# Optimization experiments

Hardware: AMD Instinct MI355X
Metric: run time of the kernel (lower is better)

## Reference

```python
import jax, jax.numpy as jnp
import numpy as np
import math
from jax import lax

B, C, H, DK, L, K, NCONV, P = 24, 128, 8, 16, 512, 7, 4, 0.1


def setup_inputs() -> dict:
    key = jax.random.key(0)
    ks = jax.random.split(key, 10)
    return {
        "x": jax.random.normal(ks[0], (B, C, L), jnp.float32),
        "dw_w": jax.random.normal(ks[1], (NCONV, C, 1, K), jnp.float32) * 0.1,
        "dw_b": jax.random.normal(ks[2], (NCONV, C), jnp.float32) * 0.1,
        "pw_w": jax.random.normal(ks[3], (NCONV, C, C, 1), jnp.float32) * 0.05,
        "pw_b": jax.random.normal(ks[4], (NCONV, C), jnp.float32) * 0.1,
        "Wq": jax.random.normal(ks[5], (H, B, DK, C), jnp.float32),
        "Wk": jax.random.normal(ks[6], (H, B, DK, C), jnp.float32),
        "Wv": jax.random.normal(ks[7], (H, B, DK, C), jnp.float32),
        "Wo": jax.random.normal(ks[8], (B, C, C), jnp.float32),
        "W": jax.random.normal(ks[9], (B, C, C), jnp.float32),
    }


def _norm(t, eps=1e-6):
    # torch: (x - mean) / (std + eps), std unbiased (ddof=1), over last (length) axis
    mean = t.mean(-1, keepdims=True)
    std = jnp.sqrt(((t - mean) ** 2).sum(-1, keepdims=True) / (t.shape[-1] - 1))
    return (t - mean) / (std + eps)


def _dropout(t, i):
    # deterministic dropout (training=True, p=0.1) with fixed per-call key
    keep = jax.random.bernoulli(jax.random.fold_in(jax.random.key(7), i), 1.0 - P, t.shape)
    return jnp.where(keep, t / (1.0 - P), jnp.zeros((), t.dtype))


def reference(x, dw_w, dw_b, pw_w, pw_b, Wq, Wk, Wv, Wo, W):
    # positional encoding: sin(sin(pos*freq + phase)) + x (note the double sin, faithful to source)
    i = np.arange(C)
    base = 10000.0 ** (-(i - (i % 2)) / C)
    freq = jnp.asarray(np.where(i % 2 == 0, base, -base), jnp.float32)
    phase = jnp.asarray(np.where(i % 2 == 0, 0.0, np.pi / 2), jnp.float32)
    pos = jnp.arange(L, dtype=jnp.float32)
    pe = jnp.sin(jnp.sin(pos[None, :] * freq[:, None] + phase[:, None]))  # (C, L)
    out = pe[None] + x
    res = out
    dn = ('NCH', 'OIH', 'NCH')
    for ci in range(NCONV):
        o = _norm(out)
        o = lax.conv_general_dilated(o, dw_w[ci], (1,), [(K // 2, K // 2)],
                                     feature_group_count=C, dimension_numbers=dn) + dw_b[ci][None, :, None]
        o = lax.conv_general_dilated(o, pw_w[ci], (1,), [(0, 0)],
                                     dimension_numbers=dn) + pw_b[ci][None, :, None]
        o = jax.nn.relu(o)
        out = _dropout(res + o, ci)
        res = out
    # self-attention (per-batch-element weight matrices, softmax over QUERY axis = torch dim=1)
    xn = _norm(out)
    q = jnp.einsum('hbkc,bcl->hbkl', Wq, xn)
    k = jnp.einsum('hbkc,bcl->hbkl', Wk, xn)
    v = jnp.einsum('hbkc,bcl->hbkl', Wv, xn)
    s = jnp.einsum('hbki,hbkj->hbij', q, k) / math.sqrt(DK)  # (H,B,L,L)
    p = jax.nn.softmax(s, axis=2)
    head = jnp.einsum('hbvi,hbij->hbvj', v, p)  # (H,B,DK,L)
    head = head.transpose(1, 0, 2, 3).reshape(B, H * DK, L)
    att = jnp.einsum('boc,bcl->bol', Wo, head)
    out = _dropout(res + att, NCONV)
    res = out
    # final per-batch projection + relu + residual
    o = jax.nn.relu(jnp.einsum('boc,bcl->bol', W, _norm(out)))
    out = _dropout(res + o, NCONV + 1)
    return out
```

## Files before the change

kernel.cpp:

```cpp
#include <hip/hip_runtime.h>
#include <stdint.h>
#include <math.h>

#define NB 24
#define NC 128
#define NH 8
#define NDK 16
#define NL 512
#define NTOT (24*128*512)

typedef float f32x4 __attribute__((ext_vector_type(4)));
typedef short s16x4 __attribute__((ext_vector_type(4)));

__device__ inline f32x4 mfma_bf16_16x16x16(s16x4 a, s16x4 b, f32x4 c) {
#if defined(__HIP_DEVICE_COMPILE__)
#if __has_builtin(__builtin_amdgcn_mfma_f32_16x16x16bf16_1k)
  return __builtin_amdgcn_mfma_f32_16x16x16bf16_1k(a, b, c, 0, 0, 0);
#else
  return __builtin_amdgcn_mfma_f32_16x16x16_bf16(a, b, c, 0, 0, 0);
#endif
#else
  (void)a; (void)b;
  return c;
#endif
}

__device__ inline unsigned short f2bf(float x) {
  uint32_t u = __float_as_uint(x);
  return (unsigned short)((u + 0x7FFFu + ((u >> 16) & 1u)) >> 16);
}
__device__ inline float bf2f(unsigned short s) {
  return __uint_as_float(((uint32_t)s) << 16);
}

__host__ __device__ inline void tf2x32(uint32_t k0, uint32_t k1, uint32_t& x0, uint32_t& x1) {
  uint32_t ks2 = k0 ^ k1 ^ 0x1BD11BDAu;
  x0 += k0; x1 += k1;
#define TF_R(r) { x0 += x1; x1 = (x1 << r) | (x1 >> (32 - r)); x1 ^= x0; }
  TF_R(13) TF_R(15) TF_R(26) TF_R(6)
  x0 += k1;  x1 += ks2 + 1u;
  TF_R(17) TF_R(29) TF_R(16) TF_R(24)
  x0 += ks2; x1 += k0 + 2u;
  TF_R(13) TF_R(15) TF_R(26) TF_R(6)
  x0 += k0;  x1 += k1 + 3u;
  TF_R(17) TF_R(29) TF_R(16) TF_R(24)
  x0 += k1;  x1 += ks2 + 4u;
  TF_R(13) TF_R(15) TF_R(26) TF_R(6)
  x0 += ks2; x1 += k0 + 5u;
#undef TF_R
}

__device__ inline float drop_scale(uint32_t k0, uint32_t k1, uint32_t idx) {
  uint32_t x0 = 0u, x1 = idx;
  tf2x32(k0, k1, x0, x1);
  uint32_t bits = x0 ^ x1;
  float u = __uint_as_float((bits >> 9) | 0x3f800000u) - 1.0f;
  return (u < 0.9f) ? (1.0f / 0.9f) : 0.0f;
}

#define S0 (4*128*128)
#define SW (24*128*128)
#define SQ (8*24*16*128)
#define oPwH 0
#define oPwL (S0)
#define oWoH (2*S0)
#define oWoL (2*S0 + SW)
#define oWH  (2*S0 + 2*SW)
#define oWL  (2*S0 + 3*SW)
#define oQH  (2*S0 + 4*SW)
#define oQL  (2*S0 + 4*SW + SQ)
#define oKH  (2*S0 + 4*SW + 2*SQ)
#define oKL  (2*S0 + 4*SW + 3*SQ)
#define oVH  (2*S0 + 4*SW + 4*SQ)
#define oVL  (2*S0 + 4*SW + 5*SQ)
#define PREP_TOT (S0 + 2*SW + 3*SQ)

__global__ __launch_bounds__(256) void prep_split_kernel(
    const float* __restrict__ pw_w, const float* __restrict__ Wo, const float* __restrict__ W,
    const float* __restrict__ Wq, const float* __restrict__ Wk, const float* __restrict__ Wv,
    unsigned short* __restrict__ ws) {
  int idx = blockIdx.x * 256 + threadIdx.x;
  const float* src; unsigned short *dh, *dl; int off;
  if (idx < S0)                { src = pw_w; dh = ws + oPwH; dl = ws + oPwL; off = idx; }
  else if (idx < S0 + SW)      { src = Wo;   dh = ws + oWoH; dl = ws + oWoL; off = idx - S0; }
  else if (idx < S0 + 2*SW)    { src = W;    dh = ws + oWH;  dl = ws + oWL;  off = idx - S0 - SW; }
  else if (idx < S0 + 2*SW + SQ)   { src = Wq; dh = ws + oQH; dl = ws + oQL; off = idx - S0 - 2*SW; }
  else if (idx < S0 + 2*SW + 2*SQ) { src = Wk; dh = ws + oKH; dl = ws + oKL; off = idx - S0 - 2*SW - SQ; }
  else                             { src = Wv; dh = ws + oVH; dl = ws + oVL; off = idx - S0 - 2*SW - 2*SQ; }
  float v = src[off];
  unsigned short hi = f2bf(v);
  dh[off] = hi;
  dl[off] = f2bf(v - bf2f(hi));
}

template<bool DO_CONV, bool ADD_PE>
__global__ __launch_bounds__(64) void norm_dw_kernel(const float* __restrict__ in,
                                                     float* __restrict__ cur_out,
                                                     unsigned short* __restrict__ oh,
                                                     unsigned short* __restrict__ ol,
                                                     const float* __restrict__ dww,
                                                     const float* __restrict__ dwb) {
  int row = blockIdx.x;
  int c = row & (NC - 1);
  int t = threadIdx.x;
  const float* rp = in + (size_t)row * NL;
  float4 v0 = ((const float4*)rp)[t * 2];
  float4 v1 = ((const float4*)rp)[t * 2 + 1];
  float xr[8] = {v0.x, v0.y, v0.z, v0.w, v1.x, v1.y, v1.z, v1.w};
  if (ADD_PE) {
    int ce = c & ~1;
    double base = exp(-(double)ce * 9.210340371976184 / 128.0);
    float freq = (c & 1) ? -(float)base : (float)base;
    float phase = (c & 1) ? (float)(M_PI / 2.0) : 0.0f;
#pragma unroll
    for (int j = 0; j < 8; ++j)
      xr[j] += sinf(sinf((float)(t * 8 + j) * freq + phase));
    float4 o0 = make_float4(xr[0], xr[1], xr[2], xr[3]);
    float4 o1 = make_float4(xr[4], xr[5], xr[6], xr[7]);
    float4* cp = (float4*)(cur_out + (size_t)row * NL);
    cp[t * 2] = o0; cp[t * 2 + 1] = o1;
  }
  float s = 0.f;
#pragma unroll
  for (int j = 0; j < 8; ++j) s += xr[j];
#pragma unroll
  for (int off = 32; off >= 1; off >>= 1) s += __shfl_xor(s, off);
  float mean = s * (1.0f / 512.0f);
  float sq = 0.f;
#pragma unroll
  for (int j = 0; j < 8; ++j) { xr[j] -= mean; sq += xr[j] * xr[j]; }
#pragma unroll
  for (int off = 32; off >= 1; off >>= 1) sq += __shfl_xor(sq, off);
  float inv = 1.0f / (sqrtf(sq * (1.0f / 511.0f)) + 1e-6f);

  size_t obase = (size_t)row * NL + t * 8;
  if (!DO_CONV) {
#pragma unroll
    for (int j = 0; j < 8; ++j) {
      float o = xr[j] * inv;
      unsigned short hi = f2bf(o);
      oh[obase + j] = hi;
      ol[obase + j] = f2bf(o - bf2f(hi));
    }
  } else {
    __shared__ float rb[NL + 6];
    if (t < 3) { rb[t] = 0.f; rb[NL + 3 + t] = 0.f; }
#pragma unroll
    for (int j = 0; j < 8; ++j) rb[3 + t * 8 + j] = xr[j] * inv;
    __syncthreads();
    float w[7];
#pragma unroll
    for (int u = 0; u < 7; ++u) w[u] = dww[c * 7 + u];
    float bias = dwb[c];
#pragma unroll
    for (int j = 0; j < 8; ++j) {
      int l = t * 8 + j;
      float o = bias;
#pragma unroll
      for (int u = 0; u < 7; ++u) o += rb[l + u] * w[u];
      unsigned short hi = f2bf(o);
      oh[obase + j] = hi;
      ol[obase + j] = f2bf(o - bf2f(hi));
    }
  }
}

template<int EPI, bool A_PER_B>
__global__ __launch_bounds__(256) void gemm_mfma_kernel(
    const unsigned short* __restrict__ AhB, const unsigned short* __restrict__ AlB,
    const unsigned short* __restrict__ XhB, const unsigned short* __restrict__ XlB,
    float* __restrict__ Y, const float* __restrict__ bias, const float* __restrict__ resid,
    uint32_t k0, uint32_t k1) {
  __shared__ unsigned short Ah[64][68], Al[64][68];
  __shared__ unsigned short Xh[64][68], Xl[64][68];
  int b  = blockIdx.z;
  int m0 = blockIdx.y * 64;
  int l0 = blockIdx.x * 64;
  int t  = threadIdx.x;
  const int lane = t & 63, w = t >> 6;
  const int g = lane >> 4, j16 = lane & 15;
  const unsigned short* Abh = AhB + (A_PER_B ? (size_t)b * NC * NC : 0);
  const unsigned short* Abl = AlB + (A_PER_B ? (size_t)b * NC * NC : 0);
  const size_t xb = (size_t)b * NC * NL;

  f32x4 acc[4] = {{0.f,0.f,0.f,0.f},{0.f,0.f,0.f,0.f},{0.f,0.f,0.f,0.f},{0.f,0.f,0.f,0.f}};

  for (int kc = 0; kc < 2; ++kc) {
#pragma unroll
    for (int i = 0; i < 4; ++i) {
      int id = t + i * 256;
      int r = id >> 4, u = (id & 15) << 2;
      *(s16x4*)&Ah[r][u] = *(const s16x4*)&Abh[(size_t)(m0 + r) * NC + kc * 64 + u];
      *(s16x4*)&Al[r][u] = *(const s16x4*)&Abl[(size_t)(m0 + r) * NC + kc * 64 + u];
    }
    {
      int n = t & 63, kq = (t >> 6) * 16;
#pragma unroll
      for (int kk = 0; kk < 16; ++kk) {
        int k = kq + kk;
        size_t src = xb + (size_t)(kc * 64 + k) * NL + l0 + n;
        Xh[n][k] = XhB[src];
        Xl[n][k] = XlB[src];
      }
    }
    __syncthreads();
#pragma unroll
    for (int ks = 0; ks < 4; ++ks) {
      int ko = ks * 16 + 4 * g;
      s16x4 a_h = *(const s16x4*)&Ah[w * 16 + j16][ko];
      s16x4 a_l = *(const s16x4*)&Al[w * 16 + j16][ko];
#pragma unroll
      for (int nt = 0; nt < 4; ++nt) {
        s16x4 x_h = *(const s16x4*)&Xh[nt * 16 + j16][ko];
        s16x4 x_l = *(const s16x4*)&Xl[nt * 16 + j16][ko];
        acc[nt] = mfma_bf16_16x16x16(a_h, x_h, acc[nt]);
        acc[nt] = mfma_bf16_16x16x16(a_l, x_h, acc[nt]);
        acc[nt] = mfma_bf16_16x16x16(a_h, x_l, acc[nt]);
      }
    }
    __syncthreads();
  }

#pragma unroll
  for (int nt = 0; nt < 4; ++nt) {
    int n = l0 + nt * 16 + j16;
#pragma unroll
    for (int r = 0; r < 4; ++r) {
      int m = m0 + w * 16 + 4 * g + r;
      float val = acc[nt][r] + ((EPI == 0) ? bias[m] : 0.0f);
      if (EPI == 0 || EPI == 2) val = fmaxf(val, 0.0f);
      size_t idx = ((size_t)b * NC + m) * NL + n;
      float v2 = resid[idx] + val;
      float ds = drop_scale(k0, k1, (uint32_t)idx);
      Y[idx] = (ds == 0.0f) ? 0.0f : (v2 / 0.9f);
    }
  }
}

__global__ __launch_bounds__(256) void qkv_mfma_kernel(
    const unsigned short* __restrict__ wsp,
    const unsigned short* __restrict__ XhB, const unsigned short* __restrict__ XlB,
    unsigned short* __restrict__ qhw, unsigned short* __restrict__ qlw,
    unsigned short* __restrict__ khw, unsigned short* __restrict__ klw,
    unsigned short* __restrict__ vbw) {
  __shared__ unsigned short Ah[64][68], Al[64][68];
  __shared__ unsigned short Xh[64][68], Xl[64][68];
  int b  = blockIdx.z;
  int m0 = blockIdx.y * 64;
  int l0 = blockIdx.x * 64;
  int t  = threadIdx.x;
  const int lane = t & 63, w = t >> 6;
  const int g = lane >> 4, j16 = lane & 15;
  const int sel = m0 >> 7;
  const unsigned short* WpH = wsp + ((sel == 0) ? oQH : (sel == 1) ? oKH : oVH);
  const unsigned short* WpL = wsp + ((sel == 0) ? oQL : (sel == 1) ? oKL : oVL);
  const size_t xb = (size_t)b * NC * NL;

  f32x4 acc[4] = {{0.f,0.f,0.f,0.f},{0.f,0.f,0.f,0.f},{0.f,0.f,0.f,0.f},{0.f,0.f,0.f,0.f}};

  for (int kc = 0; kc < 2; ++kc) {
#pragma unroll
    for (int i = 0; i < 4; ++i) {
      int id = t + i * 256;
      int r = id >> 4, u = (id & 15) << 2;
      int gr = m0 + r;
      int w_ = gr & 127, h = w_ >> 4, kk = w_ & 15;
      size_t rowoff = (((size_t)h * NB + b) * NDK + kk) * NC + kc * 64 + u;
      *(s16x4*)&Ah[r][u] = *(const s16x4*)&WpH[rowoff];
      *(s16x4*)&Al[r][u] = *(const s16x4*)&WpL[rowoff];
    }
    {
      int n = t & 63, kq = (t >> 6) * 16;
#pragma unroll
      for (int kk = 0; kk < 16; ++kk) {
        int k = kq + kk;
        size_t src = xb + (size_t)(kc * 64 + k) * NL + l0 + n;
        Xh[n][k] = XhB[src];
        Xl[n][k] = XlB[src];
      }
    }
    __syncthreads();
#pragma unroll
    for (int ks = 0; ks < 4; ++ks) {
      int ko = ks * 16 + 4 * g;
      s16x4 a_h = *(const s16x4*)&Ah[w * 16 + j16][ko];
      s16x4 a_l = *(const s16x4*)&Al[w * 16 + j16][ko];
#pragma unroll
      for (int nt = 0; nt < 4; ++nt) {
        s16x4 x_h = *(const s16x4*)&Xh[nt * 16 + j16][ko];
        s16x4 x_l = *(const s16x4*)&Xl[nt * 16 + j16][ko];
        acc[nt] = mfma_bf16_16x16x16(a_h, x_h, acc[nt]);
        acc[nt] = mfma_bf16_16x16x16(a_l, x_h, acc[nt]);
        acc[nt] = mfma_bf16_16x16x16(a_h, x_l, acc[nt]);
      }
    }
    __syncthreads();
  }

#pragma unroll
  for (int nt = 0; nt < 4; ++nt) {
    int n = l0 + nt * 16 + j16;
#pragma unroll
    for (int r = 0; r < 4; ++r) {
      int grow = m0 + w * 16 + 4 * g + r;
      int w_ = grow & 127, h = w_ >> 4, kk = w_ & 15;
      size_t idx = (((size_t)h * NB + b) * NDK + kk) * NL + n;
      float v = acc[nt][r];
      if (sel == 0) {
        float sv = v * 0.25f;
        unsigned short hi = f2bf(sv);
        qhw[idx] = hi; qlw[idx] = f2bf(sv - bf2f(hi));
      } else if (sel == 1) {
        unsigned short hi = f2bf(v);
        khw[idx] = hi; klw[idx] = f2bf(v - bf2f(hi));
      } else {
        vbw[idx] = f2bf(v);
      }
    }
  }
}

__global__ __launch_bounds__(256) void attn_kernel(const unsigned short* __restrict__ qh,
                                                   const unsigned short* __restrict__ ql,
                                                   const unsigned short* __restrict__ kh,
                                                   const unsigned short* __restrict__ kl,
                                                   const unsigned short* __restrict__ vb,
                                                   unsigned short* __restrict__ oh,
                                                   unsigned short* __restrict__ ol) {
  __shared__ unsigned short QtH[512][16], QtL[512][16];
  __shared__ unsigned short KtH[128][16], KtL[128][16];
  __shared__ unsigned short Vt[16][520];
  const int t = threadIdx.x;
  const int lane = t & 63, w = t >> 6;
  const int g = lane >> 4, j16 = lane & 15;
  const int hb = blockIdx.y, jq = blockIdx.x;
  const int j0 = jq * 128;
  const int h = hb / NB, b = hb % NB;
  const size_t kb = (size_t)hb * NDK * NL;

  for (int n = 0; n < 32; ++n) {
    int e = n * 256 + t;
    int k = e >> 9, i = e & 511;
    QtH[i][k] = qh[kb + (size_t)k * NL + i];
    QtL[i][k] = ql[kb + (size_t)k * NL + i];
  }
  for (int n = 0; n < 16; ++n) {
    int e = n * 256 + t;
    int v = e >> 8, i2 = e & 255;
    *(uint32_t*)&Vt[v][i2 * 2] = *(const uint32_t*)&vb[kb + (size_t)v * NL + i2 * 2];
  }
  for (int n = 0; n < 8; ++n) {
    int e = n * 256 + t;
    int k = e >> 7, j = e & 127;
    KtH[j][k] = kh[kb + (size_t)k * NL + j0 + j];
    KtL[j][k] = kl[kb + (size_t)k * NL + j0 + j];
  }
  __syncthreads();

  s16x4 KhiF[2], KloF[2];
#pragma unroll
  for (int q = 0; q < 2; ++q) {
    int jj = (w * 2 + q) * 16 + j16;
    KhiF[q] = *(const s16x4*)&KtH[jj][4 * g];
    KloF[q] = *(const s16x4*)&KtL[jj][4 * g];
  }

  float Mq[2] = {-INFINITY, -INFINITY};
  float lq[2] = {0.f, 0.f};
  f32x4 hC[2] = {{0.f, 0.f, 0.f, 0.f}, {0.f, 0.f, 0.f, 0.f}};

  for (int it = 0; it < 32; ++it) {
    s16x4 Qhi = *(const s16x4*)&QtH[it * 16 + j16][4 * g];
    s16x4 Qlo = *(const s16x4*)&QtL[it * 16 + j16][4 * g];
    s16x4 Vf  = *(const s16x4*)&Vt[j16][it * 16 + 4 * g];
#pragma unroll
    for (int q = 0; q < 2; ++q) {
      f32x4 S = {0.f, 0.f, 0.f, 0.f};
      S = mfma_bf16_16x16x16(Qhi, KhiF[q], S);
      S = mfma_bf16_16x16x16(Qlo, KhiF[q], S);
      S = mfma_bf16_16x16x16(Qhi, KloF[q], S);
      float tm = fmaxf(fmaxf(S[0], S[1]), fmaxf(S[2], S[3]));
      tm = fmaxf(tm, __shfl_xor(tm, 16));
      tm = fmaxf(tm, __shfl_xor(tm, 32));
      float Mn = fmaxf(Mq[q], tm);
      float corr = __expf(Mq[q] - Mn);
      Mq[q] = Mn;
      float p0 = __expf(S[0] - Mn), p1 = __expf(S[1] - Mn);
      float p2 = __expf(S[2] - Mn), p3 = __expf(S[3] - Mn);
      lq[q] = lq[q] * corr + ((p0 + p1) + (p2 + p3));
      hC[q] = hC[q] * corr;
      union { uint32_t u[2]; s16x4 s; } bp;
      bp.u[0] = (uint32_t)f2bf(p0) | ((uint32_t)f2bf(p1) << 16);
      bp.u[1] = (uint32_t)f2bf(p2) | ((uint32_t)f2bf(p3) << 16);
      hC[q] = mfma_bf16_16x16x16(Vf, bp.s, hC[q]);
    }
  }

#pragma unroll
  for (int q = 0; q < 2; ++q) {
    float l2 = lq[q] + __shfl_xor(lq[q], 16);
    float L  = l2 + __shfl_xor(l2, 32);
    float invL = 1.0f / L;
    int jglob = j0 + (w * 2 + q) * 16 + j16;
#pragma unroll
    for (int r = 0; r < 4; ++r) {
      float val = hC[q][r] * invL;
      size_t idx = ((size_t)b * NC + h * NDK + 4 * g + r) * NL + jglob;
      unsigned short hi = f2bf(val);
      oh[idx] = hi;
      ol[idx] = f2bf(val - bf2f(hi));
    }
  }
}

extern "C" void kernel_launch(void* const* d_in, const int* in_sizes, int n_in,
                              void* d_out, int out_size, void* d_ws, size_t ws_size,
                              hipStream_t stream) {
  (void)in_sizes; (void)n_in; (void)out_size; (void)ws_size;
  const float* x    = (const float*)d_in[0];
  const float* dw_w = (const float*)d_in[1];
  const float* dw_b = (const float*)d_in[2];
  const float* pw_w = (const float*)d_in[3];
  const float* pw_b = (const float*)d_in[4];
  const float* Wq   = (const float*)d_in[5];
  const float* Wk   = (const float*)d_in[6];
  const float* Wv   = (const float*)d_in[7];
  const float* Wo   = (const float*)d_in[8];
  const float* W    = (const float*)d_in[9];
  float* out = (float*)d_out;

  const size_t N = NTOT;
  float* cur = (float*)d_ws;
  unsigned short* XhB = (unsigned short*)(cur + N);
  unsigned short* XlB = XhB + N;
  unsigned short* qh  = XlB + N;
  unsigned short* ql  = qh + N;
  unsigned short* kh  = ql + N;
  unsigned short* kl  = kh + N;
  unsigned short* vb  = kl + N;
  unsigned short* wsp = vb + N;

  uint32_t fk0[6], fk1[6];
  for (int i = 0; i < 6; ++i) {
    uint32_t a = 0u, bb = (uint32_t)i;
    tf2x32(0u, 7u, a, bb);
    fk0[i] = a; fk1[i] = bb;
  }

  prep_split_kernel<<<PREP_TOT / 256, 256, 0, stream>>>(pw_w, Wo, W, Wq, Wk, Wv, wsp);

  norm_dw_kernel<true, true><<<NB * NC, 64, 0, stream>>>(x, cur, XhB, XlB, dw_w, dw_b);
  gemm_mfma_kernel<0, false><<<dim3(8, 2, NB), 256, 0, stream>>>(
      wsp + oPwH, wsp + oPwL, XhB, XlB, cur, pw_b, cur, fk0[0], fk1[0]);
  for (int ci = 1; ci < 4; ++ci) {
    norm_dw_kernel<true, false><<<NB * NC, 64, 0, stream>>>(cur, nullptr, XhB, XlB,
                                                            dw_w + ci * NC * 7, dw_b + ci * NC);
    gemm_mfma_kernel<0, false><<<dim3(8, 2, NB), 256, 0, stream>>>(
        wsp + oPwH + (size_t)ci * NC * NC, wsp + oPwL + (size_t)ci * NC * NC,
        XhB, XlB, cur, pw_b + ci * NC, cur, fk0[ci], fk1[ci]);
  }

  norm_dw_kernel<false, false><<<NB * NC, 64, 0, stream>>>(cur, nullptr, XhB, XlB, nullptr, nullptr);
  qkv_mfma_kernel<<<dim3(8, 6, NB), 256, 0, stream>>>(wsp, XhB, XlB, qh, ql, kh, kl, vb);
  attn_kernel<<<dim3(4, NH * NB), 256, 0, stream>>>(qh, ql, kh, kl, vb, XhB, XlB);
  gemm_mfma_kernel<1, true><<<dim3(8, 2, NB), 256, 0, stream>>>(
      wsp + oWoH, wsp + oWoL, XhB, XlB, cur, nullptr, cur, fk0[4], fk1[4]);

  norm_dw_kernel<false, false><<<NB * NC, 64, 0, stream>>>(cur, nullptr, XhB, XlB, nullptr, nullptr);
  gemm_mfma_kernel<2, true><<<dim3(8, 2, NB), 256, 0, stream>>>(
      wsp + oWH, wsp + oWL, XhB, XlB, out, nullptr, cur, fk0[5], fk1[5]);
}
```

Before: 186.6 us.

## Fuse layer norm and depthwise conv into GEMM prologues using partial row statistics

Removes the standalone norm/depthwise-conv kernels. Each GEMM epilogue now writes per-row partial sums and sums of squares, and the next GEMM reduces those into mean and inverse std. It then normalises, applies the depthwise conv from fp32 activations, and splits to bf16 hi/lo inside its load stage. Positional-encoding addition and the statistics are merged into the weight-prep launch, and ping-pong buffers replace in-place updates. This saves six launches and the bf16 intermediate round-trips, but the depthwise conv is recomputed redundantly across the two M-tile blocks. Variance now comes from a one-pass sum/sum-of-squares formula, which is less numerically robust.

```diff
diff --git a/kernel.cpp b/kernel.cpp
--- a/kernel.cpp
+++ b/kernel.cpp
@@ -74,105 +74,71 @@
 #define oVH  (2*S0 + 4*SW + 4*SQ)
 #define oVL  (2*S0 + 4*SW + 5*SQ)
 #define PREP_TOT (S0 + 2*SW + 3*SQ)
-
-__global__ __launch_bounds__(256) void prep_split_kernel(
+#define PREPB (PREP_TOT / 256)
+
+__global__ __launch_bounds__(256) void prep_init_kernel(
     const float* __restrict__ pw_w, const float* __restrict__ Wo, const float* __restrict__ W,
     const float* __restrict__ Wq, const float* __restrict__ Wk, const float* __restrict__ Wv,
-    unsigned short* __restrict__ ws) {
-  int idx = blockIdx.x * 256 + threadIdx.x;
-  const float* src; unsigned short *dh, *dl; int off;
-  if (idx < S0)                { src = pw_w; dh = ws + oPwH; dl = ws + oPwL; off = idx; }
-  else if (idx < S0 + SW)      { src = Wo;   dh = ws + oWoH; dl = ws + oWoL; off = idx - S0; }
-  else if (idx < S0 + 2*SW)    { src = W;    dh = ws + oWH;  dl = ws + oWL;  off = idx - S0 - SW; }
-  else if (idx < S0 + 2*SW + SQ)   { src = Wq; dh = ws + oQH; dl = ws + oQL; off = idx - S0 - 2*SW; }
-  else if (idx < S0 + 2*SW + 2*SQ) { src = Wk; dh = ws + oKH; dl = ws + oKL; off = idx - S0 - 2*SW - SQ; }
-  else                             { src = Wv; dh = ws + oVH; dl = ws + oVL; off = idx - S0 - 2*SW - 2*SQ; }
-  float v = src[off];
-  unsigned short hi = f2bf(v);
-  dh[off] = hi;
-  dl[off] = f2bf(v - bf2f(hi));
-}
-
-template<bool DO_CONV, bool ADD_PE>
-__global__ __launch_bounds__(64) void norm_dw_kernel(const float* __restrict__ in,
-                                                     float* __restrict__ cur_out,
-                                                     unsigned short* __restrict__ oh,
-                                                     unsigned short* __restrict__ ol,
-                                                     const float* __restrict__ dww,
-                                                     const float* __restrict__ dwb) {
-  int row = blockIdx.x;
+    unsigned short* __restrict__ ws,
+    const float* __restrict__ x, float* __restrict__ curA, float* __restrict__ partA) {
+  int bid = blockIdx.x;
+  if (bid < PREPB) {
+    int idx = bid * 256 + threadIdx.x;
+    const float* src; unsigned short *dh, *dl; int off;
+    if (idx < S0)                { src = pw_w; dh = ws + oPwH; dl = ws + oPwL; off = idx; }
+    else if (idx < S0 + SW)      { src = Wo;   dh = ws + oWoH; dl = ws + oWoL; off = idx - S0; }
+    else if (idx < S0 + 2*SW)    { src = W;    dh = ws + oWH;  dl = ws + oWL;  off = idx - S0 - SW; }
+    else if (idx < S0 + 2*SW + SQ)   { src = Wq; dh = ws + oQH; dl = ws + oQL; off = idx - S0 - 2*SW; }
+    else if (idx < S0 + 2*SW + 2*SQ) { src = Wk; dh = ws + oKH; dl = ws + oKL; off = idx - S0 - 2*SW - SQ; }
+    else                             { src = Wv; dh = ws + oVH; dl = ws + oVL; off = idx - S0 - 2*SW - 2*SQ; }
+    float v = src[off];
+    unsigned short hi = f2bf(v);
+    dh[off] = hi;
+    dl[off] = f2bf(v - bf2f(hi));
+    return;
+  }
+  int rb = bid - PREPB;
+  int row = rb * 4 + (threadIdx.x >> 6);
+  int t = threadIdx.x & 63;
   int c = row & (NC - 1);
-  int t = threadIdx.x;
-  const float* rp = in + (size_t)row * NL;
+  const float* rp = x + (size_t)row * NL;
   float4 v0 = ((const float4*)rp)[t * 2];
   float4 v1 = ((const float4*)rp)[t * 2 + 1];
   float xr[8] = {v0.x, v0.y, v0.z, v0.w, v1.x, v1.y, v1.z, v1.w};
-  if (ADD_PE) {
-    int ce = c & ~1;
-    double base = exp(-(double)ce * 9.210340371976184 / 128.0);
-    float freq = (c & 1) ? -(float)base : (float)base;
-    float phase = (c & 1) ? (float)(M_PI / 2.0) : 0.0f;
-#pragma unroll
-    for (int j = 0; j < 8; ++j)
-      xr[j] += sinf(sinf((float)(t * 8 + j) * freq + phase));
-    float4 o0 = make_float4(xr[0], xr[1], xr[2], xr[3]);
-    float4 o1 = make_float4(xr[4], xr[5], xr[6], xr[7]);
-    float4* cp = (float4*)(cur_out + (size_t)row * NL);
-    cp[t * 2] = o0; cp[t * 2 + 1] = o1;
-  }
-  float s = 0.f;
-#pragma unroll
-  for (int j = 0; j < 8; ++j) s += xr[j];
-#pragma unroll
-  for (int off = 32; off >= 1; off >>= 1) s += __shfl_xor(s, off);
-  float mean = s * (1.0f / 512.0f);
-  float sq = 0.f;
-#pragma unroll
-  for (int j = 0; j < 8; ++j) { xr[j] -= mean; sq += xr[j] * xr[j]; }
-#pragma unroll
-  for (int off = 32; off >= 1; off >>= 1) sq += __shfl_xor(sq, off);
-  float inv = 1.0f / (sqrtf(sq * (1.0f / 511.0f)) + 1e-6f);
-
-  size_t obase = (size_t)row * NL + t * 8;
-  if (!DO_CONV) {
-#pragma unroll
-    for (int j = 0; j < 8; ++j) {
-      float o = xr[j] * inv;
-      unsigned short hi = f2bf(o);
-      oh[obase + j] = hi;
-      ol[obase + j] = f2bf(o - bf2f(hi));
-    }
-  } else {
-    __shared__ float rb[NL + 6];
-    if (t < 3) { rb[t] = 0.f; rb[NL + 3 + t] = 0.f; }
-#pragma unroll
-    for (int j = 0; j < 8; ++j) rb[3 + t * 8 + j] = xr[j] * inv;
-    __syncthreads();
-    float w[7];
-#pragma unroll
-    for (int u = 0; u < 7; ++u) w[u] = dww[c * 7 + u];
-    float bias = dwb[c];
-#pragma unroll
-    for (int j = 0; j < 8; ++j) {
-      int l = t * 8 + j;
-      float o = bias;
-#pragma unroll
-      for (int u = 0; u < 7; ++u) o += rb[l + u] * w[u];
-      unsigned short hi = f2bf(o);
-      oh[obase + j] = hi;
-      ol[obase + j] = f2bf(o - bf2f(hi));
-    }
-  }
-}
-
-template<int EPI, bool A_PER_B>
+  int ce = c & ~1;
+  double base = exp(-(double)ce * 9.210340371976184 / 128.0);
+  float freq = (c & 1) ? -(float)base : (float)base;
+  float phase = (c & 1) ? (float)(M_PI / 2.0) : 0.0f;
+#pragma unroll
+  for (int j = 0; j < 8; ++j)
+    xr[j] += sinf(sinf((float)(t * 8 + j) * freq + phase));
+  float4* cp = (float4*)(curA + (size_t)row * NL);
+  cp[t * 2]     = make_float4(xr[0], xr[1], xr[2], xr[3]);
+  cp[t * 2 + 1] = make_float4(xr[4], xr[5], xr[6], xr[7]);
+  float s = 0.f, q = 0.f;
+#pragma unroll
+  for (int j = 0; j < 8; ++j) { s += xr[j]; q = fmaf(xr[j], xr[j], q); }
+#pragma unroll
+  for (int off = 1; off < 8; off <<= 1) { s += __shfl_xor(s, off); q += __shfl_xor(q, off); }
+  if ((t & 7) == 0) {
+    float* PD = partA + (size_t)row * 16 + (t >> 3) * 2;
+    PD[0] = s; PD[1] = q;
+  }
+}
+
+template<int STAGE, int EPI, bool A_PER_B>
 __global__ __launch_bounds__(256) void gemm_mfma_kernel(
     const unsigned short* __restrict__ AhB, const unsigned short* __restrict__ AlB,
     const unsigned short* __restrict__ XhB, const unsigned short* __restrict__ XlB,
-    float* __restrict__ Y, const float* __restrict__ bias, const float* __restrict__ resid,
+    const float* __restrict__ curStage, const float* __restrict__ partIn,
+    const float* __restrict__ dww, const float* __restrict__ dwb,
+    const float* __restrict__ bias, const float* __restrict__ resid,
+    float* __restrict__ Yout, float* __restrict__ partOut,
     uint32_t k0, uint32_t k1) {
   __shared__ unsigned short Ah[64][68], Al[64][68];
   __shared__ unsigned short Xh[64][68], Xl[64][68];
+  __shared__ float Xn[64][72];
+  __shared__ float meanS[128], invS[128];
   int b  = blockIdx.z;
   int m0 = blockIdx.y * 64;
   int l0 = blockIdx.x * 64;
@@ -183,6 +149,20 @@
   const unsigned short* Abl = AlB + (A_PER_B ? (size_t)b * NC * NC : 0);
   const size_t xb = (size_t)b * NC * NL;
 
+  if (STAGE <= 1) {
+    if (t < 128) {
+      const float* P = partIn + ((size_t)(b * NC + t)) * 16;
+      float S = 0.f, Q = 0.f;
+#pragma unroll
+      for (int i = 0; i < 8; ++i) { S += P[2 * i]; Q += P[2 * i + 1]; }
+      float mean = S * (1.0f / 512.0f);
+      float var = fmaxf(Q - S * mean, 0.f) * (1.0f / 511.0f);
+      meanS[t] = mean;
+      invS[t] = 1.0f / (sqrtf(var) + 1e-6f);
+    }
+    __syncthreads();
+  }
+
   f32x4 acc[4] = {{0.f,0.f,0.f,0.f},{0.f,0.f,0.f,0.f},{0.f,0.f,0.f,0.f},{0.f,0.f,0.f,0.f}};
 
   for (int kc = 0; kc < 2; ++kc) {
@@ -193,7 +173,35 @@
       *(s16x4*)&Ah[r][u] = *(const s16x4*)&Abh[(size_t)(m0 + r) * NC + kc * 64 + u];
       *(s16x4*)&Al[r][u] = *(const s16x4*)&Abl[(size_t)(m0 + r) * NC + kc * 64 + u];
     }
-    {
+    if (STAGE == 0) {
+      for (int idx = t; idx < 64 * 70; idx += 256) {
+        int cc = idx / 70, dl = idx - cc * 70;
+        int l = l0 + dl - 3;
+        int ch = kc * 64 + cc;
+        float v = 0.f;
+        if (l >= 0 && l < NL)
+          v = (curStage[xb + (size_t)ch * NL + l] - meanS[ch]) * invS[ch];
+        Xn[cc][dl] = v;
+      }
+      __syncthreads();
+      for (int idx = t; idx < 4096; idx += 256) {
+        int n = idx & 63, k = idx >> 6;
+        int ch = kc * 64 + k;
+        float o = dwb[ch];
+#pragma unroll
+        for (int u = 0; u < 7; ++u) o = fmaf(dww[ch * 7 + u], Xn[k][n + u], o);
+        unsigned short hi = f2bf(o);
+        Xh[n][k] = hi; Xl[n][k] = f2bf(o - bf2f(hi));
+      }
+    } else if (STAGE == 1) {
+      for (int idx = t; idx < 4096; idx += 256) {
+        int n = idx & 63, k = idx >> 6;
+        int ch = kc * 64 + k;
+        float v = (curStage[xb + (size_t)ch * NL + l0 + n] - meanS[ch]) * invS[ch];
+        unsigned short hi = f2bf(v);
+        Xh[n][k] = hi; Xl[n][k] = f2bf(v - bf2f(hi));
+      }
+    } else {
       int n = t & 63, kq = (t >> 6) * 16;
 #pragma unroll
       for (int kk = 0; kk < 16; ++kk) {
@@ -221,6 +229,7 @@
     __syncthreads();
   }
 
+  float s_[4] = {0.f,0.f,0.f,0.f}, q_[4] = {0.f,0.f,0.f,0.f};
 #pragma unroll
   for (int nt = 0; nt < 4; ++nt) {
     int n = l0 + nt * 16 + j16;
@@ -232,19 +241,35 @@
       size_t idx = ((size_t)b * NC + m) * NL + n;
       float v2 = resid[idx] + val;
       float ds = drop_scale(k0, k1, (uint32_t)idx);
-      Y[idx] = (ds == 0.0f) ? 0.0f : (v2 / 0.9f);
+      float yv = (ds == 0.0f) ? 0.0f : (v2 / 0.9f);
+      Yout[idx] = yv;
+      if (EPI < 2) { s_[r] += yv; q_[r] = fmaf(yv, yv, q_[r]); }
+    }
+  }
+  if (EPI < 2) {
+#pragma unroll
+    for (int r = 0; r < 4; ++r) {
+      float s = s_[r], q = q_[r];
+#pragma unroll
+      for (int off = 1; off < 16; off <<= 1) { s += __shfl_xor(s, off); q += __shfl_xor(q, off); }
+      if (j16 == 0) {
+        int m = m0 + w * 16 + 4 * g + r;
+        float* PD = partOut + ((size_t)(b * NC + m)) * 16 + (size_t)blockIdx.x * 2;
+        PD[0] = s; PD[1] = q;
+      }
     }
   }
 }
 
 __global__ __launch_bounds__(256) void qkv_mfma_kernel(
     const unsigned short* __restrict__ wsp,
-    const unsigned short* __restrict__ XhB, const unsigned short* __restrict__ XlB,
+    const float* __restrict__ curStage, const float* __restrict__ partIn,
     unsigned short* __restrict__ qhw, unsigned short* __restrict__ qlw,
     unsigned short* __restrict__ khw, unsigned short* __restrict__ klw,
     unsigned short* __restrict__ vbw) {
   __shared__ unsigned short Ah[64][68], Al[64][68];
   __shared__ unsigned short Xh[64][68], Xl[64][68];
+  __shared__ float meanS[128], invS[128];
   int b  = blockIdx.z;
   int m0 = blockIdx.y * 64;
   int l0 = blockIdx.x * 64;
@@ -256,6 +281,18 @@
   const unsigned short* WpL = wsp + ((sel == 0) ? oQL : (sel == 1) ? oKL : oVL);
   const size_t xb = (size_t)b * NC * NL;
 
+  if (t < 128) {
+    const float* P = partIn + ((size_t)(b * NC + t)) * 16;
+    float S = 0.f, Q = 0.f;
+#pragma unroll
+    for (int i = 0; i < 8; ++i) { S += P[2 * i]; Q += P[2 * i + 1]; }
+    float mean = S * (1.0f / 512.0f);
+    float var = fmaxf(Q - S * mean, 0.f) * (1.0f / 511.0f);
+    meanS[t] = mean;
+    invS[t] = 1.0f / (sqrtf(var) + 1e-6f);
+  }
+  __syncthreads();
+
   f32x4 acc[4] = {{0.f,0.f,0.f,0.f},{0.f,0.f,0.f,0.f},{0.f,0.f,0.f,0.f},{0.f,0.f,0.f,0.f}};
 
   for (int kc = 0; kc < 2; ++kc) {
@@ -269,15 +306,12 @@
       *(s16x4*)&Ah[r][u] = *(const s16x4*)&WpH[rowoff];
       *(s16x4*)&Al[r][u] = *(const s16x4*)&WpL[rowoff];
     }
-    {
-      int n = t & 63, kq = (t >> 6) * 16;
-#pragma unroll
-      for (int kk = 0; kk < 16; ++kk) {
-        int k = kq + kk;
-        size_t src = xb + (size_t)(kc * 64 + k) * NL + l0 + n;
-        Xh[n][k] = XhB[src];
-        Xl[n][k] = XlB[src];
-      }
+    for (int idx = t; idx < 4096; idx += 256) {
+      int n = idx & 63, k = idx >> 6;
+      int ch = kc * 64 + k;
+      float v = (curStage[xb + (size_t)ch * NL + l0 + n] - meanS[ch]) * invS[ch];
+      unsigned short hi = f2bf(v);
+      Xh[n][k] = hi; Xl[n][k] = f2bf(v - bf2f(hi));
     }
     __syncthreads();
 #pragma unroll
@@ -430,8 +464,11 @@
   float* out = (float*)d_out;
 
   const size_t N = NTOT;
-  float* cur = (float*)d_ws;
-  unsigned short* XhB = (unsigned short*)(cur + N);
+  float* curA  = (float*)d_ws;
+  float* curB  = curA + N;
+  float* partA = curB + N;
+  float* partB = partA + 3072 * 16;
+  unsigned short* XhB = (unsigned short*)(partB + 3072 * 16);
   unsigned short* XlB = XhB + N;
   unsigned short* qh  = XlB + N;
   unsigned short* ql  = qh + N;
@@ -447,26 +484,26 @@
     fk0[i] = a; fk1[i] = bb;
   }
 
-  prep_split_kernel<<<PREP_TOT / 256, 256, 0, stream>>>(pw_w, Wo, W, Wq, Wk, Wv, wsp);
-
-  norm_dw_kernel<true, true><<<NB * NC, 64, 0, stream>>>(x, cur, XhB, XlB, dw_w, dw_b);
-  gemm_mfma_kernel<0, false><<<dim3(8, 2, NB), 256, 0, stream>>>(
-      wsp + oPwH, wsp + oPwL, XhB, XlB, cur, pw_b, cur, fk0[0], fk1[0]);
-  for (int ci = 1; ci < 4; ++ci) {
-    norm_dw_kernel<true, false><<<NB * NC, 64, 0, stream>>>(cur, nullptr, XhB, XlB,
-                                                            dw_w + ci * NC * 7, dw_b + ci * NC);
-    gemm_mfma_kernel<0, false><<<dim3(8, 2, NB), 256, 0, stream>>>(
+  prep_init_kernel<<<PREPB + 768, 256, 0, stream>>>(pw_w, Wo, W, Wq, Wk, Wv, wsp, x, curA, partA);
+
+  float* cin = curA;  float* pin = partA;
+  float* cout = curB; float* pout = partB;
+  for (int ci = 0; ci < 4; ++ci) {
+    gemm_mfma_kernel<0, 0, false><<<dim3(8, 2, NB), 256, 0, stream>>>(
         wsp + oPwH + (size_t)ci * NC * NC, wsp + oPwL + (size_t)ci * NC * NC,
-        XhB, XlB, cur, pw_b + ci * NC, cur, fk0[ci], fk1[ci]);
-  }
-
-  norm_dw_kernel<false, false><<<NB * NC, 64, 0, stream>>>(cur, nullptr, XhB, XlB, nullptr, nullptr);
-  qkv_mfma_kernel<<<dim3(8, 6, NB), 256, 0, stream>>>(wsp, XhB, XlB, qh, ql, kh, kl, vb);
+        nullptr, nullptr, cin, pin,
+        dw_w + (size_t)ci * NC * 7, dw_b + (size_t)ci * NC,
+        pw_b + (size_t)ci * NC, cin, cout, pout, fk0[ci], fk1[ci]);
+    float* tc = cin; cin = cout; cout = tc;
+    float* tp = pin; pin = pout; pout = tp;
+  }
+
+  qkv_mfma_kernel<<<dim3(8, 6, NB), 256, 0, stream>>>(wsp, cin, pin, qh, ql, kh, kl, vb);
   attn_kernel<<<dim3(4, NH * NB), 256, 0, stream>>>(qh, ql, kh, kl, vb, XhB, XlB);
-  gemm_mfma_kernel<1, true><<<dim3(8, 2, NB), 256, 0, stream>>>(
-      wsp + oWoH, wsp + oWoL, XhB, XlB, cur, nullptr, cur, fk0[4], fk1[4]);
-
-  norm_dw_kernel<false, false><<<NB * NC, 64, 0, stream>>>(cur, nullptr, XhB, XlB, nullptr, nullptr);
-  gemm_mfma_kernel<2, true><<<dim3(8, 2, NB), 256, 0, stream>>>(
-      wsp + oWH, wsp + oWL, XhB, XlB, out, nullptr, cur, fk0[5], fk1[5]);
-}
+  gemm_mfma_kernel<2, 1, true><<<dim3(8, 2, NB), 256, 0, stream>>>(
+      wsp + oWoH, wsp + oWoL, XhB, XlB, nullptr, nullptr,
+      nullptr, nullptr, nullptr, cin, cout, pout, fk0[4], fk1[4]);
+  gemm_mfma_kernel<1, 2, true><<<dim3(8, 2, NB), 256, 0, stream>>>(
+      wsp + oWH, wsp + oWL, nullptr, nullptr, cout, pout,
+      nullptr, nullptr, nullptr, cout, out, nullptr, fk0[5], fk1[5]);
+}
```

After: 226.6 us. 21.4% more time.

## Stage full-K activation tile once per block and loop over output row tiles

Applied to the files above, without the earlier changes.

The GEMM and QKV kernels now load the whole 128-deep activation slab into shared memory once and iterate over all M tiles inside the block, instead of launching one block per M tile that reloads the same X data. The attention kernel likewise loops over the four key chunks inside one block per head/batch, loading Q and V once. This removes redundant global reads and transposed scalar LDS stores, but cuts the grid size sharply (192 blocks for GEMMs and attention), reducing parallelism and latency hiding on a large GPU.

```diff
diff --git a/kernel.cpp b/kernel.cpp
--- a/kernel.cpp
+++ b/kernel.cpp
@@ -171,10 +171,9 @@
     const unsigned short* __restrict__ XhB, const unsigned short* __restrict__ XlB,
     float* __restrict__ Y, const float* __restrict__ bias, const float* __restrict__ resid,
     uint32_t k0, uint32_t k1) {
-  __shared__ unsigned short Ah[64][68], Al[64][68];
-  __shared__ unsigned short Xh[64][68], Xl[64][68];
-  int b  = blockIdx.z;
-  int m0 = blockIdx.y * 64;
+  __shared__ unsigned short Xh[64][132], Xl[64][132];
+  __shared__ unsigned short Ah[64][68],  Al[64][68];
+  int b  = blockIdx.y;
   int l0 = blockIdx.x * 64;
   int t  = threadIdx.x;
   const int lane = t & 63, w = t >> 6;
@@ -183,56 +182,58 @@
   const unsigned short* Abl = AlB + (A_PER_B ? (size_t)b * NC * NC : 0);
   const size_t xb = (size_t)b * NC * NL;
 
-  f32x4 acc[4] = {{0.f,0.f,0.f,0.f},{0.f,0.f,0.f,0.f},{0.f,0.f,0.f,0.f},{0.f,0.f,0.f,0.f}};
-
-  for (int kc = 0; kc < 2; ++kc) {
-#pragma unroll
-    for (int i = 0; i < 4; ++i) {
-      int id = t + i * 256;
-      int r = id >> 4, u = (id & 15) << 2;
-      *(s16x4*)&Ah[r][u] = *(const s16x4*)&Abh[(size_t)(m0 + r) * NC + kc * 64 + u];
-      *(s16x4*)&Al[r][u] = *(const s16x4*)&Abl[(size_t)(m0 + r) * NC + kc * 64 + u];
-    }
-    {
-      int n = t & 63, kq = (t >> 6) * 16;
-#pragma unroll
-      for (int kk = 0; kk < 16; ++kk) {
-        int k = kq + kk;
-        size_t src = xb + (size_t)(kc * 64 + k) * NL + l0 + n;
-        Xh[n][k] = XhB[src];
-        Xl[n][k] = XlB[src];
-      }
-    }
-    __syncthreads();
-#pragma unroll
-    for (int ks = 0; ks < 4; ++ks) {
-      int ko = ks * 16 + 4 * g;
-      s16x4 a_h = *(const s16x4*)&Ah[w * 16 + j16][ko];
-      s16x4 a_l = *(const s16x4*)&Al[w * 16 + j16][ko];
-#pragma unroll
-      for (int nt = 0; nt < 4; ++nt) {
-        s16x4 x_h = *(const s16x4*)&Xh[nt * 16 + j16][ko];
-        s16x4 x_l = *(const s16x4*)&Xl[nt * 16 + j16][ko];
-        acc[nt] = mfma_bf16_16x16x16(a_h, x_h, acc[nt]);
-        acc[nt] = mfma_bf16_16x16x16(a_l, x_h, acc[nt]);
-        acc[nt] = mfma_bf16_16x16x16(a_h, x_l, acc[nt]);
-      }
-    }
-    __syncthreads();
-  }
-
-#pragma unroll
-  for (int nt = 0; nt < 4; ++nt) {
-    int n = l0 + nt * 16 + j16;
-#pragma unroll
-    for (int r = 0; r < 4; ++r) {
-      int m = m0 + w * 16 + 4 * g + r;
-      float val = acc[nt][r] + ((EPI == 0) ? bias[m] : 0.0f);
-      if (EPI == 0 || EPI == 2) val = fmaxf(val, 0.0f);
-      size_t idx = ((size_t)b * NC + m) * NL + n;
-      float v2 = resid[idx] + val;
-      float ds = drop_scale(k0, k1, (uint32_t)idx);
-      Y[idx] = (ds == 0.0f) ? 0.0f : (v2 / 0.9f);
+  {
+    int n = t & 63, kq = (t >> 6) * 32;
+    for (int kk = 0; kk < 32; ++kk) {
+      int k = kq + kk;
+      size_t src = xb + (size_t)k * NL + l0 + n;
+      Xh[n][k] = XhB[src];
+      Xl[n][k] = XlB[src];
+    }
+  }
+
+  for (int mt = 0; mt < 2; ++mt) {
+    int m0 = mt * 64;
+    f32x4 acc[4] = {{0.f,0.f,0.f,0.f},{0.f,0.f,0.f,0.f},{0.f,0.f,0.f,0.f},{0.f,0.f,0.f,0.f}};
+    for (int kc = 0; kc < 2; ++kc) {
+      __syncthreads();
+#pragma unroll
+      for (int i = 0; i < 4; ++i) {
+        int id = t + i * 256;
+        int r = id >> 4, u = (id & 15) << 2;
+        *(s16x4*)&Ah[r][u] = *(const s16x4*)&Abh[(size_t)(m0 + r) * NC + kc * 64 + u];
+        *(s16x4*)&Al[r][u] = *(const s16x4*)&Abl[(size_t)(m0 + r) * NC + kc * 64 + u];
+      }
+      __syncthreads();
+#pragma unroll
+      for (int ks = 0; ks < 4; ++ks) {
+        int ka = ks * 16 + 4 * g;
+        int kx = kc * 64 + ka;
+        s16x4 a_h = *(const s16x4*)&Ah[w * 16 + j16][ka];
+        s16x4 a_l = *(const s16x4*)&Al[w * 16 + j16][ka];
+#pragma unroll
+        for (int nt = 0; nt < 4; ++nt) {
+          s16x4 x_h = *(const s16x4*)&Xh[nt * 16 + j16][kx];
+          s16x4 x_l = *(const s16x4*)&Xl[nt * 16 + j16][kx];
+          acc[nt] = mfma_bf16_16x16x16(a_h, x_h, acc[nt]);
+          acc[nt] = mfma_bf16_16x16x16(a_l, x_h, acc[nt]);
+          acc[nt] = mfma_bf16_16x16x16(a_h, x_l, acc[nt]);
+        }
+      }
+    }
+#pragma unroll
+    for (int nt = 0; nt < 4; ++nt) {
+      int n = l0 + nt * 16 + j16;
+#pragma unroll
+      for (int r = 0; r < 4; ++r) {
+        int m = m0 + w * 16 + 4 * g + r;
+        float val = acc[nt][r] + ((EPI == 0) ? bias[m] : 0.0f);
+        if (EPI == 0 || EPI == 2) val = fmaxf(val, 0.0f);
+        size_t idx = ((size_t)b * NC + m) * NL + n;
+        float v2 = resid[idx] + val;
+        float ds = drop_scale(k0, k1, (uint32_t)idx);
+        Y[idx] = (ds == 0.0f) ? 0.0f : (v2 / 0.9f);
+      }
     }
   }
 }
@@ -243,78 +244,79 @@
     unsigned short* __restrict__ qhw, unsigned short* __restrict__ qlw,
     unsigned short* __restrict__ khw, unsigned short* __restrict__ klw,
     unsigned short* __restrict__ vbw) {
-  __shared__ unsigned short Ah[64][68], Al[64][68];
-  __shared__ unsigned short Xh[64][68], Xl[64][68];
-  int b  = blockIdx.z;
-  int m0 = blockIdx.y * 64;
+  __shared__ unsigned short Xh[64][132], Xl[64][132];
+  __shared__ unsigned short Ah[64][68],  Al[64][68];
+  int b  = blockIdx.y;
   int l0 = blockIdx.x * 64;
   int t  = threadIdx.x;
   const int lane = t & 63, w = t >> 6;
   const int g = lane >> 4, j16 = lane & 15;
-  const int sel = m0 >> 7;
-  const unsigned short* WpH = wsp + ((sel == 0) ? oQH : (sel == 1) ? oKH : oVH);
-  const unsigned short* WpL = wsp + ((sel == 0) ? oQL : (sel == 1) ? oKL : oVL);
   const size_t xb = (size_t)b * NC * NL;
 
-  f32x4 acc[4] = {{0.f,0.f,0.f,0.f},{0.f,0.f,0.f,0.f},{0.f,0.f,0.f,0.f},{0.f,0.f,0.f,0.f}};
-
-  for (int kc = 0; kc < 2; ++kc) {
-#pragma unroll
-    for (int i = 0; i < 4; ++i) {
-      int id = t + i * 256;
-      int r = id >> 4, u = (id & 15) << 2;
-      int gr = m0 + r;
-      int w_ = gr & 127, h = w_ >> 4, kk = w_ & 15;
-      size_t rowoff = (((size_t)h * NB + b) * NDK + kk) * NC + kc * 64 + u;
-      *(s16x4*)&Ah[r][u] = *(const s16x4*)&WpH[rowoff];
-      *(s16x4*)&Al[r][u] = *(const s16x4*)&WpL[rowoff];
-    }
-    {
-      int n = t & 63, kq = (t >> 6) * 16;
-#pragma unroll
-      for (int kk = 0; kk < 16; ++kk) {
-        int k = kq + kk;
-        size_t src = xb + (size_t)(kc * 64 + k) * NL + l0 + n;
-        Xh[n][k] = XhB[src];
-        Xl[n][k] = XlB[src];
-      }
-    }
-    __syncthreads();
-#pragma unroll
-    for (int ks = 0; ks < 4; ++ks) {
-      int ko = ks * 16 + 4 * g;
-      s16x4 a_h = *(const s16x4*)&Ah[w * 16 + j16][ko];
-      s16x4 a_l = *(const s16x4*)&Al[w * 16 + j16][ko];
-#pragma unroll
-      for (int nt = 0; nt < 4; ++nt) {
-        s16x4 x_h = *(const s16x4*)&Xh[nt * 16 + j16][ko];
-        s16x4 x_l = *(const s16x4*)&Xl[nt * 16 + j16][ko];
-        acc[nt] = mfma_bf16_16x16x16(a_h, x_h, acc[nt]);
-        acc[nt] = mfma_bf16_16x16x16(a_l, x_h, acc[nt]);
-        acc[nt] = mfma_bf16_16x16x16(a_h, x_l, acc[nt]);
-      }
-    }
-    __syncthreads();
-  }
-
-#pragma unroll
-  for (int nt = 0; nt < 4; ++nt) {
-    int n = l0 + nt * 16 + j16;
-#pragma unroll
-    for (int r = 0; r < 4; ++r) {
-      int grow = m0 + w * 16 + 4 * g + r;
-      int w_ = grow & 127, h = w_ >> 4, kk = w_ & 15;
-      size_t idx = (((size_t)h * NB + b) * NDK + kk) * NL + n;
-      float v = acc[nt][r];
-      if (sel == 0) {
-        float sv = v * 0.25f;
-        unsigned short hi = f2bf(sv);
-        qhw[idx] = hi; qlw[idx] = f2bf(sv - bf2f(hi));
-      } else if (sel == 1) {
-        unsigned short hi = f2bf(v);
-        khw[idx] = hi; klw[idx] = f2bf(v - bf2f(hi));
-      } else {
-        vbw[idx] = f2bf(v);
+  {
+    int n = t & 63, kq = (t >> 6) * 32;
+    for (int kk = 0; kk < 32; ++kk) {
+      int k = kq + kk;
+      size_t src = xb + (size_t)k * NL + l0 + n;
+      Xh[n][k] = XhB[src];
+      Xl[n][k] = XlB[src];
+    }
+  }
+
+  for (int mt = 0; mt < 6; ++mt) {
+    int m0 = mt * 64;
+    const int sel = m0 >> 7;
+    const unsigned short* WpH = wsp + ((sel == 0) ? oQH : (sel == 1) ? oKH : oVH);
+    const unsigned short* WpL = wsp + ((sel == 0) ? oQL : (sel == 1) ? oKL : oVL);
+    f32x4 acc[4] = {{0.f,0.f,0.f,0.f},{0.f,0.f,0.f,0.f},{0.f,0.f,0.f,0.f},{0.f,0.f,0.f,0.f}};
+    for (int kc = 0; kc < 2; ++kc) {
+      __syncthreads();
+#pragma unroll
+      for (int i = 0; i < 4; ++i) {
+        int id = t + i * 256;
+        int r = id >> 4, u = (id & 15) << 2;
+        int gr = m0 + r;
+        int w_ = gr & 127, h = w_ >> 4, kk = w_ & 15;
+        size_t rowoff = (((size_t)h * NB + b) * NDK + kk) * NC + kc * 64 + u;
+        *(s16x4*)&Ah[r][u] = *(const s16x4*)&WpH[rowoff];
+        *(s16x4*)&Al[r][u] = *(const s16x4*)&WpL[rowoff];
+      }
+      __syncthreads();
+#pragma unroll
+      for (int ks = 0; ks < 4; ++ks) {
+        int ka = ks * 16 + 4 * g;
+        int kx = kc * 64 + ka;
+        s16x4 a_h = *(const s16x4*)&Ah[w * 16 + j16][ka];
+        s16x4 a_l = *(const s16x4*)&Al[w * 16 + j16][ka];
+#pragma unroll
+        for (int nt = 0; nt < 4; ++nt) {
+          s16x4 x_h = *(const s16x4*)&Xh[nt * 16 + j16][kx];
+          s16x4 x_l = *(const s16x4*)&Xl[nt * 16 + j16][kx];
+          acc[nt] = mfma_bf16_16x16x16(a_h, x_h, acc[nt]);
+          acc[nt] = mfma_bf16_16x16x16(a_l, x_h, acc[nt]);
+          acc[nt] = mfma_bf16_16x16x16(a_h, x_l, acc[nt]);
+        }
+      }
+    }
+#pragma unroll
+    for (int nt = 0; nt < 4; ++nt) {
+      int n = l0 + nt * 16 + j16;
+#pragma unroll
+      for (int r = 0; r < 4; ++r) {
+        int grow = m0 + w * 16 + 4 * g + r;
+        int w_ = grow & 127, h = w_ >> 4, kk = w_ & 15;
+        size_t idx = (((size_t)h * NB + b) * NDK + kk) * NL + n;
+        float v = acc[nt][r];
+        if (sel == 0) {
+          float sv = v * 0.25f;
+          unsigned short hi = f2bf(sv);
+          qhw[idx] = hi; qlw[idx] = f2bf(sv - bf2f(hi));
+        } else if (sel == 1) {
+          unsigned short hi = f2bf(v);
+          khw[idx] = hi; klw[idx] = f2bf(v - bf2f(hi));
+        } else {
+          vbw[idx] = f2bf(v);
+        }
       }
     }
   }
@@ -333,8 +335,7 @@
   const int t = threadIdx.x;
   const int lane = t & 63, w = t >> 6;
   const int g = lane >> 4, j16 = lane & 15;
-  const int hb = blockIdx.y, jq = blockIdx.x;
-  const int j0 = jq * 128;
+  const int hb = blockIdx.x;
   const int h = hb / NB, b = hb % NB;
   const size_t kb = (size_t)hb * NDK * NL;
 
@@ -349,66 +350,71 @@
     int v = e >> 8, i2 = e & 255;
     *(uint32_t*)&Vt[v][i2 * 2] = *(const uint32_t*)&vb[kb + (size_t)v * NL + i2 * 2];
   }
-  for (int n = 0; n < 8; ++n) {
-    int e = n * 256 + t;
-    int k = e >> 7, j = e & 127;
-    KtH[j][k] = kh[kb + (size_t)k * NL + j0 + j];
-    KtL[j][k] = kl[kb + (size_t)k * NL + j0 + j];
-  }
-  __syncthreads();
-
-  s16x4 KhiF[2], KloF[2];
-#pragma unroll
-  for (int q = 0; q < 2; ++q) {
-    int jj = (w * 2 + q) * 16 + j16;
-    KhiF[q] = *(const s16x4*)&KtH[jj][4 * g];
-    KloF[q] = *(const s16x4*)&KtL[jj][4 * g];
-  }
-
-  float Mq[2] = {-INFINITY, -INFINITY};
-  float lq[2] = {0.f, 0.f};
-  f32x4 hC[2] = {{0.f, 0.f, 0.f, 0.f}, {0.f, 0.f, 0.f, 0.f}};
-
-  for (int it = 0; it < 32; ++it) {
-    s16x4 Qhi = *(const s16x4*)&QtH[it * 16 + j16][4 * g];
-    s16x4 Qlo = *(const s16x4*)&QtL[it * 16 + j16][4 * g];
-    s16x4 Vf  = *(const s16x4*)&Vt[j16][it * 16 + 4 * g];
+
+  for (int jq = 0; jq < 4; ++jq) {
+    const int j0 = jq * 128;
+    __syncthreads();
+    for (int n = 0; n < 8; ++n) {
+      int e = n * 256 + t;
+      int k = e >> 7, j = e & 127;
+      KtH[j][k] = kh[kb + (size_t)k * NL + j0 + j];
+      KtL[j][k] = kl[kb + (size_t)k * NL + j0 + j];
+    }
+    __syncthreads();
+
+    s16x4 KhiF[2], KloF[2];
 #pragma unroll
     for (int q = 0; q < 2; ++q) {
-      f32x4 S = {0.f, 0.f, 0.f, 0.f};
-      S = mfma_bf16_16x16x16(Qhi, KhiF[q], S);
-      S = mfma_bf16_16x16x16(Qlo, KhiF[q], S);
-      S = mfma_bf16_16x16x16(Qhi, KloF[q], S);
-      float tm = fmaxf(fmaxf(S[0], S[1]), fmaxf(S[2], S[3]));
-      tm = fmaxf(tm, __shfl_xor(tm, 16));
-      tm = fmaxf(tm, __shfl_xor(tm, 32));
-      float Mn = fmaxf(Mq[q], tm);
-      float corr = __expf(Mq[q] - Mn);
-      Mq[q] = Mn;
-      float p0 = __expf(S[0] - Mn), p1 = __expf(S[1] - Mn);
-      float p2 = __expf(S[2] - Mn), p3 = __expf(S[3] - Mn);
-      lq[q] = lq[q] * corr + ((p0 + p1) + (p2 + p3));
-      hC[q] = hC[q] * corr;
-      union { uint32_t u[2]; s16x4 s; } bp;
-      bp.u[0] = (uint32_t)f2bf(p0) | ((uint32_t)f2bf(p1) << 16);
-      bp.u[1] = (uint32_t)f2bf(p2) | ((uint32_t)f2bf(p3) << 16);
-      hC[q] = mfma_bf16_16x16x16(Vf, bp.s, hC[q]);
-    }
-  }
-
-#pragma unroll
-  for (int q = 0; q < 2; ++q) {
-    float l2 = lq[q] + __shfl_xor(lq[q], 16);
-    float L  = l2 + __shfl_xor(l2, 32);
-    float invL = 1.0f / L;
-    int jglob = j0 + (w * 2 + q) * 16 + j16;
-#pragma unroll
-    for (int r = 0; r < 4; ++r) {
-      float val = hC[q][r] * invL;
-      size_t idx = ((size_t)b * NC + h * NDK + 4 * g + r) * NL + jglob;
-      unsigned short hi = f2bf(val);
-      oh[idx] = hi;
-      ol[idx] = f2bf(val - bf2f(hi));
+      int jj = (w * 2 + q) * 16 + j16;
+      KhiF[q] = *(const s16x4*)&KtH[jj][4 * g];
+      KloF[q] = *(const s16x4*)&KtL[jj][4 * g];
+    }
+
+    float Mq[2] = {-INFINITY, -INFINITY};
+    float lq[2] = {0.f, 0.f};
+    f32x4 hC[2] = {{0.f, 0.f, 0.f, 0.f}, {0.f, 0.f, 0.f, 0.f}};
+
+    for (int it = 0; it < 32; ++it) {
+      s16x4 Qhi = *(const s16x4*)&QtH[it * 16 + j16][4 * g];
+      s16x4 Qlo = *(const s16x4*)&QtL[it * 16 + j16][4 * g];
+      s16x4 Vf  = *(const s16x4*)&Vt[j16][it * 16 + 4 * g];
+#pragma unroll
+      for (int q = 0; q < 2; ++q) {
+        f32x4 S = {0.f, 0.f, 0.f, 0.f};
+        S = mfma_bf16_16x16x16(Qhi, KhiF[q], S);
+        S = mfma_bf16_16x16x16(Qlo, KhiF[q], S);
+        S = mfma_bf16_16x16x16(Qhi, KloF[q], S);
+        float tm = fmaxf(fmaxf(S[0], S[1]), fmaxf(S[2], S[3]));
+        tm = fmaxf(tm, __shfl_xor(tm, 16));
+        tm = fmaxf(tm, __shfl_xor(tm, 32));
+        float Mn = fmaxf(Mq[q], tm);
+        float corr = __expf(Mq[q] - Mn);
+        Mq[q] = Mn;
+        float p0 = __expf(S[0] - Mn), p1 = __expf(S[1] - Mn);
+        float p2 = __expf(S[2] - Mn), p3 = __expf(S[3] - Mn);
+        lq[q] = lq[q] * corr + ((p0 + p1) + (p2 + p3));
+        hC[q] = hC[q] * corr;
+        union { uint32_t u[2]; s16x4 s; } bp;
+        bp.u[0] = (uint32_t)f2bf(p0) | ((uint32_t)f2bf(p1) << 16);
+        bp.u[1] = (uint32_t)f2bf(p2) | ((uint32_t)f2bf(p3) << 16);
+        hC[q] = mfma_bf16_16x16x16(Vf, bp.s, hC[q]);
+      }
+    }
+
+#pragma unroll
+    for (int q = 0; q < 2; ++q) {
+      float l2 = lq[q] + __shfl_xor(lq[q], 16);
+      float L  = l2 + __shfl_xor(l2, 32);
+      float invL = 1.0f / L;
+      int jglob = j0 + (w * 2 + q) * 16 + j16;
+#pragma unroll
+      for (int r = 0; r < 4; ++r) {
+        float val = hC[q][r] * invL;
+        size_t idx = ((size_t)b * NC + h * NDK + 4 * g + r) * NL + jglob;
+        unsigned short hi = f2bf(val);
+        oh[idx] = hi;
+        ol[idx] = f2bf(val - bf2f(hi));
+      }
     }
   }
 }
@@ -450,23 +456,23 @@
   prep_split_kernel<<<PREP_TOT / 256, 256, 0, stream>>>(pw_w, Wo, W, Wq, Wk, Wv, wsp);
 
   norm_dw_kernel<true, true><<<NB * NC, 64, 0, stream>>>(x, cur, XhB, XlB, dw_w, dw_b);
-  gemm_mfma_kernel<0, false><<<dim3(8, 2, NB), 256, 0, stream>>>(
+  gemm_mfma_kernel<0, false><<<dim3(8, NB), 256, 0, stream>>>(
       wsp + oPwH, wsp + oPwL, XhB, XlB, cur, pw_b, cur, fk0[0], fk1[0]);
   for (int ci = 1; ci < 4; ++ci) {
     norm_dw_kernel<true, false><<<NB * NC, 64, 0, stream>>>(cur, nullptr, XhB, XlB,
                                                             dw_w + ci * NC * 7, dw_b + ci * NC);
-    gemm_mfma_kernel<0, false><<<dim3(8, 2, NB), 256, 0, stream>>>(
+    gemm_mfma_kernel<0, false><<<dim3(8, NB), 256, 0, stream>>>(
         wsp + oPwH + (size_t)ci * NC * NC, wsp + oPwL + (size_t)ci * NC * NC,
         XhB, XlB, cur, pw_b + ci * NC, cur, fk0[ci], fk1[ci]);
   }
 
   norm_dw_kernel<false, false><<<NB * NC, 64, 0, stream>>>(cur, nullptr, XhB, XlB, nullptr, nullptr);
-  qkv_mfma_kernel<<<dim3(8, 6, NB), 256, 0, stream>>>(wsp, XhB, XlB, qh, ql, kh, kl, vb);
-  attn_kernel<<<dim3(4, NH * NB), 256, 0, stream>>>(qh, ql, kh, kl, vb, XhB, XlB);
-  gemm_mfma_kernel<1, true><<<dim3(8, 2, NB), 256, 0, stream>>>(
+  qkv_mfma_kernel<<<dim3(8, NB), 256, 0, stream>>>(wsp, XhB, XlB, qh, ql, kh, kl, vb);
+  attn_kernel<<<NH * NB, 256, 0, stream>>>(qh, ql, kh, kl, vb, XhB, XlB);
+  gemm_mfma_kernel<1, true><<<dim3(8, NB), 256, 0, stream>>>(
       wsp + oWoH, wsp + oWoL, XhB, XlB, cur, nullptr, cur, fk0[4], fk1[4]);
 
   norm_dw_kernel<false, false><<<NB * NC, 64, 0, stream>>>(cur, nullptr, XhB, XlB, nullptr, nullptr);
-  gemm_mfma_kernel<2, true><<<dim3(8, 2, NB), 256, 0, stream>>>(
+  gemm_mfma_kernel<2, true><<<dim3(8, NB), 256, 0, stream>>>(
       wsp + oWH, wsp + oWL, XhB, XlB, out, nullptr, cur, fk0[5], fk1[5]);
 }
```

Result: slower. 246.5 us (+32.1%).
